# Optimization experiments

Measured on AMD Instinct MI355X. Metric: run time of the kernel, lower is better.

## Reference

```python
import jax, jax.numpy as jnp
import numpy as np

B, N, H, G = 32, 8192, 128, 10
EPS = 1e-10
THRESHOLD = 8.0
LOG_2PI = float(np.log(2.0 * np.pi))


def _init_head(key, h, g):
    k1, k2 = jax.random.split(key)
    s1 = 1.0 / np.sqrt(h)
    w1 = jax.random.uniform(k1, (h, h), jnp.float32, -s1, s1)
    b1 = jnp.zeros((h,), jnp.float32)
    w2 = jax.random.uniform(k2, (h, g), jnp.float32, -s1, s1)
    b2 = jnp.zeros((g,), jnp.float32)
    return w1, b1, w2, b2


def setup_inputs() -> dict:
    key = jax.random.key(0)
    kf, kd, kpi, ksig, kmu = jax.random.split(key, 5)
    features = jax.random.normal(kf, (B, N, H), jnp.float32)
    dist = jax.random.uniform(kd, (B, N), jnp.float32) * 10.0  # distances in [0, 10)
    dist_mask = jnp.ones((B, N), dtype=bool)
    w1_pi, b1_pi, w2_pi, b2_pi = _init_head(kpi, H, G)
    w1_sig, b1_sig, w2_sig, b2_sig = _init_head(ksig, H, G)
    w1_mu, b1_mu, w2_mu, b2_mu = _init_head(kmu, H, G)
    return {
        'features': features, 'dist': dist, 'dist_mask': dist_mask,
        'w1_pi': w1_pi, 'b1_pi': b1_pi, 'w2_pi': w2_pi, 'b2_pi': b2_pi,
        'w1_sig': w1_sig, 'b1_sig': b1_sig, 'w2_sig': w2_sig, 'b2_sig': b2_sig,
        'w1_mu': w1_mu, 'b1_mu': b1_mu, 'w2_mu': w2_mu, 'b2_mu': b2_mu,
    }


def _head(x, w1, b1, w2, b2):
    # NonLinearHead: Linear -> relu -> Linear
    return jax.nn.relu(x @ w1 + b1) @ w2 + b2


def reference(features, dist, dist_mask,
              w1_pi, b1_pi, w2_pi, b2_pi,
              w1_sig, b1_sig, w2_sig, b2_sig,
              w1_mu, b1_mu, w2_mu, b2_mu):
    mask = dist_mask & (dist <= THRESHOLD)  # [B,N]
    pi = jax.nn.softmax(_head(features, w1_pi, b1_pi, w2_pi, b2_pi), -1)      # [B,N,G]
    sigma = jax.nn.elu(_head(features, w1_sig, b1_sig, w2_sig, b2_sig)) + 1.4  # [B,N,G]
    mu = jax.nn.elu(_head(features, w1_mu, b1_mu, w2_mu, b2_mu)) + 1.0         # [B,N,G]
    d = dist[..., None]  # [B,N,1]
    # Normal(mu, sigma).log_prob(d)
    loglik = -0.5 * jnp.square((d - mu) / sigma) - jnp.log(sigma) - 0.5 * LOG_2PI
    candidate_loss = -jax.scipy.special.logsumexp(jnp.log(pi + EPS) + loglik, axis=-1)  # [B,N]
    maskf = mask.astype(candidate_loss.dtype)
    loss = jnp.sum(candidate_loss * maskf) / jnp.maximum(jnp.sum(maskf), 1.0)
    prob = jnp.sum(jnp.exp(loglik) * pi, axis=-1) / (dist * dist + EPS)  # [B,N]
    score = jnp.sum(prob * maskf, axis=-1)  # [B]
    return score, loss, pi, mu, sigma
```

## Files before the change

kernel.cpp:

```cpp
#include <hip/hip_runtime.h>
#include <hip/hip_bf16.h>
#include <math.h>

#define B_   32
#define N_   8192
#define H_   128
#define G_   10
#define TOKS (B_*N_)
#define THREADS 512
#define WAVES 8
#define NITER 4
#define TPB 1024
#define LDW 136

typedef short bf16x8 __attribute__((ext_vector_type(8)));
typedef short bf16x4 __attribute__((ext_vector_type(4)));
typedef float f32x4 __attribute__((ext_vector_type(4)));

#define WS_IMG_OFF 256
#define IMG_BYTES  119232
#define IMG_INSTS  117

struct __align__(16) SMem {
  short w1s[3][H_][LDW];
  short w2s[3][16][LDW];
  float b1s[3][H_];
  float b2s[3][16];
  float red[WAVES][3];
  char  pad[640];
};

__device__ __forceinline__ short f2bf(float f) {
  __hip_bfloat16 h = __float2bfloat16(f);
  union { __hip_bfloat16 h; short s; } u; u.h = h;
  return u.s;
}

__device__ __forceinline__ void async_copy16(void* lds_uniform, const void* gsrc_perlane) {
  __builtin_amdgcn_global_load_lds(
      (const __attribute__((address_space(1))) unsigned int*)gsrc_perlane,
      (__attribute__((address_space(3))) unsigned int*)lds_uniform,
      16, 0, 0);
}

__global__ __launch_bounds__(64) void init_kernel(float* out, float* ws) {
  int t = threadIdx.x;
  if (t < 33) out[t] = 0.0f;
  if (t < 2)  ws[t]  = 0.0f;
}

__global__ __launch_bounds__(64) void fin_kernel(float* out, const float* ws) {
  if (threadIdx.x == 0) out[32] = ws[0] / fmaxf(ws[1], 1.0f);
}

__global__ __launch_bounds__(256) void prep_kernel(
    const float* __restrict__ w1_0, const float* __restrict__ b1_0,
    const float* __restrict__ w2_0, const float* __restrict__ b2_0,
    const float* __restrict__ w1_1, const float* __restrict__ b1_1,
    const float* __restrict__ w2_1, const float* __restrict__ b2_1,
    const float* __restrict__ w1_2, const float* __restrict__ b1_2,
    const float* __restrict__ w2_2, const float* __restrict__ b2_2,
    short* __restrict__ img) {
  const float* w1p[3] = {w1_0, w1_1, w1_2};
  const float* w2p[3] = {w2_0, w2_1, w2_2};
  const float* b1p[3] = {b1_0, b1_1, b1_2};
  const float* b2p[3] = {b2_0, b2_1, b2_2};
  int t = blockIdx.x * 256 + threadIdx.x;
  int stride = gridDim.x * 256;
  for (int idx = t; idx < 3*H_*LDW; idx += stride) {
    int h = idx / (H_*LDW), rem = idx - h*(H_*LDW);
    int j = rem / LDW, i = rem - j*LDW;
    img[idx] = (i < H_) ? f2bf(w1p[h][i*H_ + j]) : (short)0;
  }
  for (int idx = t; idx < 3*16*LDW; idx += stride) {
    int h = idx / (16*LDW), rem = idx - h*(16*LDW);
    int g = rem / LDW, k = rem - g*LDW;
    img[3*H_*LDW + idx] = (g < G_ && k < H_) ? f2bf(w2p[h][k*G_ + g]) : (short)0;
  }
  float* bimg = (float*)(img + 3*H_*LDW + 3*16*LDW);
  if (t < 3*H_ + 3*16) {
    if (t < 3*H_) { int h = t >> 7, j = t & 127; bimg[t] = b1p[h][j]; }
    else { int i2 = t - 3*H_; int h = i2 >> 4, g = i2 & 15;
           bimg[t] = (g < G_) ? b2p[h][g] : 0.0f; }
  }
}

template<int PREP>
__global__ __launch_bounds__(THREADS, 2)
void rtm_main(const float* __restrict__ feat,
              const float* __restrict__ dist,
              const int* __restrict__ dmask,
              const float* __restrict__ img,
              const float* __restrict__ w1_0, const float* __restrict__ b1_0,
              const float* __restrict__ w2_0, const float* __restrict__ b2_0,
              const float* __restrict__ w1_1, const float* __restrict__ b1_1,
              const float* __restrict__ w2_1, const float* __restrict__ b2_1,
              const float* __restrict__ w1_2, const float* __restrict__ b1_2,
              const float* __restrict__ w2_2, const float* __restrict__ b2_2,
              float* __restrict__ out, float* __restrict__ ws) {
  __shared__ SMem sm;

  const int tid  = threadIdx.x;
  const int wave = tid >> 6;
  const int lane = tid & 63;
  const int q  = lane >> 4;
  const int lg = lane & 15;
  const long wbase = (long)blockIdx.x * TPB + (long)wave * (32*NITER);

  float4 fv[2][8];
  float dpre[2]; int mpre[2];
#pragma unroll
  for (int mt = 0; mt < 2; ++mt) {
    const float* fr = feat + (wbase + mt*16 + lg) * (long)H_;
#pragma unroll
    for (int c = 0; c < 4; ++c) {
      const float4* p = reinterpret_cast<const float4*>(fr + c*32 + q*8);
      fv[mt][2*c]   = p[0];
      fv[mt][2*c+1] = p[1];
    }
    dpre[mt] = dist[wbase + mt*16 + lg];
    mpre[mt] = dmask[wbase + mt*16 + lg];
  }

  if constexpr (PREP) {
    char* smb = (char*)&sm;
    const char* gimg = (const char*)img;
    for (int i = wave; i < IMG_INSTS; i += WAVES)
      async_copy16(smb + i*1024, gimg + i*1024 + lane*16);
  } else {
    const float* w1p[3] = {w1_0, w1_1, w1_2};
    const float* w2p[3] = {w2_0, w2_1, w2_2};
    const float* b1p[3] = {b1_0, b1_1, b1_2};
    const float* b2p[3] = {b2_0, b2_1, b2_2};
    for (int h = 0; h < 3; ++h) {
      for (int idx = tid; idx < H_*H_; idx += THREADS) {
        int i = idx >> 7, j = idx & 127;
        sm.w1s[h][j][i] = f2bf(w1p[h][idx]);
      }
      for (int idx = tid; idx < 16*H_; idx += THREADS) {
        int g = idx >> 7, k = idx & 127;
        sm.w2s[h][g][k] = (g < G_) ? f2bf(w2p[h][(size_t)k*G_ + g]) : (short)0;
      }
      if (tid < H_) sm.b1s[h][tid] = b1p[h][tid];
      if (tid < 16) sm.b2s[h][tid] = (tid < G_) ? b2p[h][tid] : 0.0f;
    }
  }

  bf16x8 a1[2][4];
#pragma unroll
  for (int mt = 0; mt < 2; ++mt)
#pragma unroll
    for (int c = 0; c < 4; ++c) {
      float4 lo = fv[mt][2*c], hi = fv[mt][2*c+1];
      bf16x8 a;
      a[0]=f2bf(lo.x); a[1]=f2bf(lo.y); a[2]=f2bf(lo.z); a[3]=f2bf(lo.w);
      a[4]=f2bf(hi.x); a[5]=f2bf(hi.y); a[6]=f2bf(hi.z); a[7]=f2bf(hi.w);
      a1[mt][c] = a;
    }

  __syncthreads();

  float* out_score = out;
  float* out_pi = out + 33;
  float* out_mu = out + 33 + (size_t)TOKS*G_;
  float* out_sg = out + 33 + 2*(size_t)TOKS*G_;
  const float HLOG2PI = 0.91893853320467274f;
  const bool v0 = (q*4+0) < G_, v1 = (q*4+1) < G_, v2 = (q*4+2) < G_, v3 = (q*4+3) < G_;

  float accP = 0.f, accL = 0.f, accC = 0.f;

#pragma unroll
  for (int s = 0; s < NITER; ++s) {
    float dnx[2]; int mnx[2];
    if (s + 1 < NITER) {
#pragma unroll
      for (int mt = 0; mt < 2; ++mt) {
        const float* fr = feat + (wbase + (s+1)*32 + mt*16 + lg) * (long)H_;
#pragma unroll
        for (int c = 0; c < 4; ++c) {
          const float4* p = reinterpret_cast<const float4*>(fr + c*32 + q*8);
          fv[mt][2*c]   = p[0];
          fv[mt][2*c+1] = p[1];
        }
        dnx[mt] = dist[wbase + (s+1)*32 + mt*16 + lg];
        mnx[mt] = dmask[wbase + (s+1)*32 + mt*16 + lg];
      }
    }

    f32x4 lgt[3][2];
#pragma unroll
    for (int h = 0; h < 3; ++h) {
      bf16x4 w2fr[8];
#pragma unroll
      for (int nt = 0; nt < 8; ++nt)
        w2fr[nt] = *reinterpret_cast<const bf16x4*>(&sm.w2s[h][lg][nt*16 + q*4]);

      f32x4 acc[2][8];
#pragma unroll
      for (int mt = 0; mt < 2; ++mt)
#pragma unroll
        for (int nt = 0; nt < 8; ++nt) acc[mt][nt] = (f32x4){0.f,0.f,0.f,0.f};
#pragma unroll
      for (int c = 0; c < 4; ++c) {
#pragma unroll
        for (int nt = 0; nt < 8; ++nt) {
          bf16x8 wfr = *reinterpret_cast<const bf16x8*>(&sm.w1s[h][nt*16 + lg][c*32 + q*8]);
          acc[0][nt] = __builtin_amdgcn_mfma_f32_16x16x32_bf16(wfr, a1[0][c], acc[0][nt], 0, 0, 0);
          acc[1][nt] = __builtin_amdgcn_mfma_f32_16x16x32_bf16(wfr, a1[1][c], acc[1][nt], 0, 0, 0);
        }
      }
#pragma unroll
      for (int mt = 0; mt < 2; ++mt) {
        f32x4 lacc = (f32x4){0.f,0.f,0.f,0.f};
#pragma unroll
        for (int nt = 0; nt < 8; ++nt) {
          f32x4 b1v = *reinterpret_cast<const f32x4*>(&sm.b1s[h][nt*16 + q*4]);
          bf16x4 pkv;
#pragma unroll
          for (int r = 0; r < 4; ++r)
            pkv[r] = f2bf(fmaxf(acc[mt][nt][r] + b1v[r], 0.0f));
          lacc = __builtin_amdgcn_mfma_f32_16x16x16bf16_1k(w2fr[nt], pkv, lacc, 0, 0, 0);
        }
        f32x4 b2v = *reinterpret_cast<const f32x4*>(&sm.b2s[h][q*4]);
        lgt[h][mt] = lacc + b2v;
      }
    }

#pragma unroll
    for (int mt = 0; mt < 2; ++mt) {
      long tok = wbase + s*32 + mt*16 + lg;
      float d  = dpre[mt];
      bool  mk = (mpre[mt] != 0) && (d <= 8.0f);
      f32x4 LP = lgt[0][mt], LS = lgt[1][mt], LM = lgt[2][mt];

      float vm = v0 ? LP[0] : -INFINITY;
      if (v1) vm = fmaxf(vm, LP[1]);
      if (v2) vm = fmaxf(vm, LP[2]);
      if (v3) vm = fmaxf(vm, LP[3]);
      vm = fmaxf(vm, __shfl_xor(vm, 16));
      vm = fmaxf(vm, __shfl_xor(vm, 32));
      float e0 = v0 ? __expf(LP[0]-vm) : 0.f;
      float e1 = v1 ? __expf(LP[1]-vm) : 0.f;
      float e2 = v2 ? __expf(LP[2]-vm) : 0.f;
      float e3 = v3 ? __expf(LP[3]-vm) : 0.f;
      float ssum = e0+e1+e2+e3;
      ssum += __shfl_xor(ssum, 16);
      ssum += __shfl_xor(ssum, 32);
      float inv = 1.0f / ssum;
      float pi[4] = {e0*inv, e1*inv, e2*inv, e3*inv};

      float sg[4], mu[4], ll[4];
#pragma unroll
      for (int r = 0; r < 4; ++r) {
        sg[r] = (LS[r] > 0.f) ? (LS[r] + 1.4f) : (__expf(LS[r]) + 0.4f);
        mu[r] = (LM[r] > 0.f) ? (LM[r] + 1.0f) : __expf(LM[r]);
        float z = (d - mu[r]) / sg[r];
        ll[r] = -0.5f*z*z - __logf(sg[r]) - HLOG2PI;
      }

      if (q*4 < G_) {
        size_t o = (size_t)tok*G_ + q*4;
        *reinterpret_cast<float2*>(&out_pi[o]) = make_float2(pi[0], pi[1]);
        *reinterpret_cast<float2*>(&out_mu[o]) = make_float2(mu[0], mu[1]);
        *reinterpret_cast<float2*>(&out_sg[o]) = make_float2(sg[0], sg[1]);
        if (q*4+2 < G_) {
          *reinterpret_cast<float2*>(&out_pi[o+2]) = make_float2(pi[2], pi[3]);
          *reinterpret_cast<float2*>(&out_mu[o+2]) = make_float2(mu[2], mu[3]);
          *reinterpret_cast<float2*>(&out_sg[o+2]) = make_float2(sg[2], sg[3]);
        }
      }

      float a0 = v0 ? (__logf(pi[0]+1e-10f) + ll[0]) : -INFINITY;
      float a1x= v1 ? (__logf(pi[1]+1e-10f) + ll[1]) : -INFINITY;
      float a2 = v2 ? (__logf(pi[2]+1e-10f) + ll[2]) : -INFINITY;
      float a3 = v3 ? (__logf(pi[3]+1e-10f) + ll[3]) : -INFINITY;
      float m2 = fmaxf(fmaxf(a0,a1x), fmaxf(a2,a3));
      m2 = fmaxf(m2, __shfl_xor(m2, 16));
      m2 = fmaxf(m2, __shfl_xor(m2, 32));
      float s2 = (v0?__expf(a0-m2):0.f) + (v1?__expf(a1x-m2):0.f)
               + (v2?__expf(a2-m2):0.f) + (v3?__expf(a3-m2):0.f);
      s2 += __shfl_xor(s2, 16);
      s2 += __shfl_xor(s2, 32);
      float closs = -(m2 + __logf(s2));

      float s3 = (v0?__expf(ll[0])*pi[0]:0.f) + (v1?__expf(ll[1])*pi[1]:0.f)
               + (v2?__expf(ll[2])*pi[2]:0.f) + (v3?__expf(ll[3])*pi[3]:0.f);
      s3 += __shfl_xor(s3, 16);
      s3 += __shfl_xor(s3, 32);
      float prob = s3 / (d*d + 1e-10f);

      if (lane < 16 && mk) { accP += prob; accL += closs; accC += 1.f; }
    }

    if (s + 1 < NITER) {
#pragma unroll
      for (int mt = 0; mt < 2; ++mt) {
#pragma unroll
        for (int c = 0; c < 4; ++c) {
          float4 lo = fv[mt][2*c], hi = fv[mt][2*c+1];
          bf16x8 a;
          a[0]=f2bf(lo.x); a[1]=f2bf(lo.y); a[2]=f2bf(lo.z); a[3]=f2bf(lo.w);
          a[4]=f2bf(hi.x); a[5]=f2bf(hi.y); a[6]=f2bf(hi.z); a[7]=f2bf(hi.w);
          a1[mt][c] = a;
        }
        dpre[mt] = dnx[mt]; mpre[mt] = mnx[mt];
      }
    }
  }

  accP += __shfl_xor(accP, 1); accP += __shfl_xor(accP, 2);
  accP += __shfl_xor(accP, 4); accP += __shfl_xor(accP, 8);
  accL += __shfl_xor(accL, 1); accL += __shfl_xor(accL, 2);
  accL += __shfl_xor(accL, 4); accL += __shfl_xor(accL, 8);
  accC += __shfl_xor(accC, 1); accC += __shfl_xor(accC, 2);
  accC += __shfl_xor(accC, 4); accC += __shfl_xor(accC, 8);
  if (lane == 0) { sm.red[wave][0] = accP; sm.red[wave][1] = accL; sm.red[wave][2] = accC; }
  __syncthreads();
  if (tid == 0) {
    float sP = 0.f, sL = 0.f, sC = 0.f;
    for (int w = 0; w < WAVES; ++w) { sP += sm.red[w][0]; sL += sm.red[w][1]; sC += sm.red[w][2]; }
    int b = blockIdx.x >> 3;
    atomicAdd(&out_score[b], sP);
    atomicAdd(&ws[0], sL);
    atomicAdd(&ws[1], sC);
  }
}

extern "C" void kernel_launch(void* const* d_in, const int* in_sizes, int n_in,
                              void* d_out, int out_size, void* d_ws, size_t ws_size,
                              hipStream_t stream) {
  const float* feat = (const float*)d_in[0];
  const float* dist = (const float*)d_in[1];
  const int* dmask = (const int*)d_in[2];
  float* out = (float*)d_out;
  float* ws  = (float*)d_ws;

  hipLaunchKernelGGL(init_kernel, dim3(1), dim3(64), 0, stream, out, ws);

  bool prep_ok = (ws_size >= (size_t)(WS_IMG_OFF + IMG_INSTS*1024));
  if (prep_ok) {
    short* img = (short*)((char*)d_ws + WS_IMG_OFF);
    hipLaunchKernelGGL(prep_kernel, dim3(116), dim3(256), 0, stream,
        (const float*)d_in[3],  (const float*)d_in[4],  (const float*)d_in[5],  (const float*)d_in[6],
        (const float*)d_in[7],  (const float*)d_in[8],  (const float*)d_in[9],  (const float*)d_in[10],
        (const float*)d_in[11], (const float*)d_in[12], (const float*)d_in[13], (const float*)d_in[14],
        img);
    hipLaunchKernelGGL((rtm_main<1>), dim3(TOKS/TPB), dim3(THREADS), 0, stream,
        feat, dist, dmask, (const float*)img,
        (const float*)d_in[3],  (const float*)d_in[4],  (const float*)d_in[5],  (const float*)d_in[6],
        (const float*)d_in[7],  (const float*)d_in[8],  (const float*)d_in[9],  (const float*)d_in[10],
        (const float*)d_in[11], (const float*)d_in[12], (const float*)d_in[13], (const float*)d_in[14],
        out, ws);
  } else {
    hipLaunchKernelGGL((rtm_main<0>), dim3(TOKS/TPB), dim3(THREADS), 0, stream,
        feat, dist, dmask, (const float*)nullptr,
        (const float*)d_in[3],  (const float*)d_in[4],  (const float*)d_in[5],  (const float*)d_in[6],
        (const float*)d_in[7],  (const float*)d_in[8],  (const float*)d_in[9],  (const float*)d_in[10],
        (const float*)d_in[11], (const float*)d_in[12], (const float*)d_in[13], (const float*)d_in[14],
        out, ws);
  }

  hipLaunchKernelGGL(fin_kernel, dim3(1), dim3(64), 0, stream, out, ws);
}
```

Measured before the change: 65.85 us.

## Reuse logsumexp terms for prob, prelayout W2 fragments, split second-layer accumulators

```diff
diff --git a/kernel.cpp b/kernel.cpp
--- a/kernel.cpp
+++ b/kernel.cpp
@@ -18,12 +18,14 @@
 typedef float f32x4 __attribute__((ext_vector_type(4)));
 
 #define WS_IMG_OFF 256
-#define IMG_BYTES  119232
-#define IMG_INSTS  117
+#define IMG_W2   (3*H_*LDW)
+#define IMG_BF   (IMG_W2 + 3*8*64*4)
+#define IMG_BYTES (IMG_BF*2 + 3*H_*4 + 3*16*4)
+#define IMG_INSTS 116
 
 struct __align__(16) SMem {
   short w1s[3][H_][LDW];
-  short w2s[3][16][LDW];
+  short w2f[3][8][64][4];
   float b1s[3][H_];
   float b2s[3][16];
   float red[WAVES][3];
@@ -72,12 +74,17 @@
     int j = rem / LDW, i = rem - j*LDW;
     img[idx] = (i < H_) ? f2bf(w1p[h][i*H_ + j]) : (short)0;
   }
-  for (int idx = t; idx < 3*16*LDW; idx += stride) {
-    int h = idx / (16*LDW), rem = idx - h*(16*LDW);
-    int g = rem / LDW, k = rem - g*LDW;
-    img[3*H_*LDW + idx] = (g < G_ && k < H_) ? f2bf(w2p[h][k*G_ + g]) : (short)0;
-  }
-  float* bimg = (float*)(img + 3*H_*LDW + 3*16*LDW);
+  for (int idx = t; idx < 3*8*64; idx += stride) {
+    int h = idx / 512, rem = idx - h*512;
+    int nt = rem >> 6, ln = rem & 63;
+    int qq = ln >> 4, lg = ln & 15;
+#pragma unroll
+    for (int e = 0; e < 4; ++e) {
+      int k = nt*16 + qq*4 + e;
+      img[IMG_W2 + idx*4 + e] = (lg < G_) ? f2bf(w2p[h][k*G_ + lg]) : (short)0;
+    }
+  }
+  float* bimg = (float*)(img + IMG_BF);
   if (t < 3*H_ + 3*16) {
     if (t < 3*H_) { int h = t >> 7, j = t & 127; bimg[t] = b1p[h][j]; }
     else { int i2 = t - 3*H_; int h = i2 >> 4, g = i2 & 15;
@@ -137,9 +144,14 @@
         int i = idx >> 7, j = idx & 127;
         sm.w1s[h][j][i] = f2bf(w1p[h][idx]);
       }
-      for (int idx = tid; idx < 16*H_; idx += THREADS) {
-        int g = idx >> 7, k = idx & 127;
-        sm.w2s[h][g][k] = (g < G_) ? f2bf(w2p[h][(size_t)k*G_ + g]) : (short)0;
+      for (int idx = tid; idx < 8*64; idx += THREADS) {
+        int nt = idx >> 6, ln = idx & 63;
+        int qq = ln >> 4, lgg = ln & 15;
+#pragma unroll
+        for (int e = 0; e < 4; ++e) {
+          int k = nt*16 + qq*4 + e;
+          sm.w2f[h][nt][ln][e] = (lgg < G_) ? f2bf(w2p[h][k*G_ + lgg]) : (short)0;
+        }
       }
       if (tid < H_) sm.b1s[h][tid] = b1p[h][tid];
       if (tid < 16) sm.b2s[h][tid] = (tid < G_) ? b2p[h][tid] : 0.0f;
@@ -193,7 +205,7 @@
       bf16x4 w2fr[8];
 #pragma unroll
       for (int nt = 0; nt < 8; ++nt)
-        w2fr[nt] = *reinterpret_cast<const bf16x4*>(&sm.w2s[h][lg][nt*16 + q*4]);
+        w2fr[nt] = *reinterpret_cast<const bf16x4*>(sm.w2f[h][nt][lane]);
 
       f32x4 acc[2][8];
 #pragma unroll
@@ -211,7 +223,8 @@
       }
 #pragma unroll
       for (int mt = 0; mt < 2; ++mt) {
-        f32x4 lacc = (f32x4){0.f,0.f,0.f,0.f};
+        f32x4 lacc0 = (f32x4){0.f,0.f,0.f,0.f};
+        f32x4 lacc1 = (f32x4){0.f,0.f,0.f,0.f};
 #pragma unroll
         for (int nt = 0; nt < 8; ++nt) {
           f32x4 b1v = *reinterpret_cast<const f32x4*>(&sm.b1s[h][nt*16 + q*4]);
@@ -219,10 +232,13 @@
 #pragma unroll
           for (int r = 0; r < 4; ++r)
             pkv[r] = f2bf(fmaxf(acc[mt][nt][r] + b1v[r], 0.0f));
-          lacc = __builtin_amdgcn_mfma_f32_16x16x16bf16_1k(w2fr[nt], pkv, lacc, 0, 0, 0);
+          if (nt & 1)
+            lacc1 = __builtin_amdgcn_mfma_f32_16x16x16bf16_1k(w2fr[nt], pkv, lacc1, 0, 0, 0);
+          else
+            lacc0 = __builtin_amdgcn_mfma_f32_16x16x16bf16_1k(w2fr[nt], pkv, lacc0, 0, 0, 0);
         }
         f32x4 b2v = *reinterpret_cast<const f32x4*>(&sm.b2s[h][q*4]);
-        lgt[h][mt] = lacc + b2v;
+        lgt[h][mt] = lacc0 + lacc1 + b2v;
       }
     }
 
@@ -246,6 +262,7 @@
       float ssum = e0+e1+e2+e3;
       ssum += __shfl_xor(ssum, 16);
       ssum += __shfl_xor(ssum, 32);
+      float lss = __logf(ssum);
       float inv = 1.0f / ssum;
       float pi[4] = {e0*inv, e1*inv, e2*inv, e3*inv};
 
@@ -270,10 +287,11 @@
         }
       }
 
-      float a0 = v0 ? (__logf(pi[0]+1e-10f) + ll[0]) : -INFINITY;
-      float a1x= v1 ? (__logf(pi[1]+1e-10f) + ll[1]) : -INFINITY;
-      float a2 = v2 ? (__logf(pi[2]+1e-10f) + ll[2]) : -INFINITY;
-      float a3 = v3 ? (__logf(pi[3]+1e-10f) + ll[3]) : -INFINITY;
+      float base = -vm - lss;
+      float a0 = v0 ? (LP[0] + base + ll[0]) : -INFINITY;
+      float a1x= v1 ? (LP[1] + base + ll[1]) : -INFINITY;
+      float a2 = v2 ? (LP[2] + base + ll[2]) : -INFINITY;
+      float a3 = v3 ? (LP[3] + base + ll[3]) : -INFINITY;
       float m2 = fmaxf(fmaxf(a0,a1x), fmaxf(a2,a3));
       m2 = fmaxf(m2, __shfl_xor(m2, 16));
       m2 = fmaxf(m2, __shfl_xor(m2, 32));
@@ -282,12 +300,7 @@
       s2 += __shfl_xor(s2, 16);
       s2 += __shfl_xor(s2, 32);
       float closs = -(m2 + __logf(s2));
-
-      float s3 = (v0?__expf(ll[0])*pi[0]:0.f) + (v1?__expf(ll[1])*pi[1]:0.f)
-               + (v2?__expf(ll[2])*pi[2]:0.f) + (v3?__expf(ll[3])*pi[3]:0.f);
-      s3 += __shfl_xor(s3, 16);
-      s3 += __shfl_xor(s3, 32);
-      float prob = s3 / (d*d + 1e-10f);
+      float prob = s2 * __expf(m2) / (d*d + 1e-10f);
 
       if (lane < 16 && mk) { accP += prob; accL += closs; accC += 1.f; }
     }
```

After: 67.29 us. 1.02x slower.
